# Kernel tuning notes

Measured on AMD Instinct MI355X. Metric: run time of the kernel, lower is better.

## Reference

```python
import jax, jax.numpy as jnp
import numpy as np
from jax import lax

K = 7          # neighborhood kernel size
NUM_HEADS = 4
EPS = 1e-5


def layernorm(x, w, b):
    mu = x.mean(-1, keepdims=True)
    var = ((x - mu) ** 2).mean(-1, keepdims=True)
    return (x - mu) * lax.rsqrt(var + EPS) * w + b


def window_idx(n, k):
    # NATTEN border behavior: window is shifted (not shrunk) at edges.
    start = jnp.clip(jnp.arange(n) - k // 2, 0, n - k)
    return start[:, None] + jnp.arange(k)  # [n, k]


def neighborhood_attention(x, qkv_w, qkv_b, rpb, proj_w, proj_b):
    B, H, W, C = x.shape
    nh, k = NUM_HEADS, K
    hd = C // nh
    scale = hd ** -0.5
    qkv = (x @ qkv_w + qkv_b).reshape(B, H, W, 3, nh, hd)
    q = jnp.transpose(qkv[:, :, :, 0], (0, 3, 1, 2, 4)) * scale  # [B,nh,H,W,hd]
    kk = jnp.transpose(qkv[:, :, :, 1], (0, 3, 1, 2, 4))
    vv = jnp.transpose(qkv[:, :, :, 2], (0, 3, 1, 2, 4))

    ri = window_idx(H, k)  # [H,k]
    ci = window_idx(W, k)  # [W,k]

    def gather(t):  # [B,nh,H,W,hd] -> [B,nh,H,W,k,k,hd]
        t = t[:, :, ri]           # [B,nh,H,k,W,hd]
        t = t[:, :, :, :, ci]     # [B,nh,H,k,W,k,hd]
        return jnp.transpose(t, (0, 1, 2, 4, 3, 5, 6))

    k_nb = gather(kk)
    v_nb = gather(vv).reshape(B, nh, H, W, k * k, hd)

    attn = jnp.einsum('bnhwd,bnhwijd->bnhwij', q, k_nb)  # [B,nh,H,W,k,k]

    # relative positional bias, rpb: [nh, 2k-1, 2k-1]
    br = ri - jnp.arange(H)[:, None] + (k - 1)  # [H,k] in [0, 2k-2]
    bc = ci - jnp.arange(W)[:, None] + (k - 1)  # [W,k]
    bias = rpb[:, br]                 # [nh,H,k,2k-1]
    bias = bias[:, :, :, bc]          # [nh,H,k,W,k]
    bias = jnp.transpose(bias, (0, 1, 3, 2, 4))  # [nh,H,W,k,k]

    attn = jax.nn.softmax((attn + bias[None]).reshape(B, nh, H, W, k * k), axis=-1)
    out = jnp.einsum('bnhwl,bnhwld->bnhwd', attn, v_nb)
    out = jnp.transpose(out, (0, 2, 3, 1, 4)).reshape(B, H, W, C)
    return out @ proj_w + proj_b


def mlp(x, w1, b1, w2, b2):
    return jax.nn.gelu(x @ w1 + b1, approximate=False) @ w2 + b2


def nat_block_forward(x, norm1_w, norm1_b, qkv_w, qkv_b, rpb, proj_w, proj_b,
                      norm2_w, norm2_b, fc1_w, fc1_b, fc2_w, fc2_b,
                      conv_w, dnorm_w, dnorm_b):
    depth = norm1_w.shape[0]
    for i in range(depth):
        h = layernorm(x, norm1_w[i], norm1_b[i])
        h = neighborhood_attention(h, qkv_w[i], qkv_b[i], rpb[i], proj_w[i], proj_b[i])
        x = x + h
        x = x + mlp(layernorm(x, norm2_w[i], norm2_b[i]),
                    fc1_w[i], fc1_b[i], fc2_w[i], fc2_b[i])
    # ConvDownsampler: 3x3 stride-2 conv (no bias) + LayerNorm, channels-last
    y = lax.conv_general_dilated(x, conv_w, (2, 2), ((1, 1), (1, 1)),
                                 dimension_numbers=('NHWC', 'HWIO', 'NHWC'))
    y = layernorm(y, dnorm_w, dnorm_b)
    return (y, x)


def setup_inputs() -> dict:
    key = jax.random.key(0)
    ks = jax.random.split(key, 12)
    B, H, W, C = 2, 56, 56, 128
    depth, nh, k = 2, NUM_HEADS, K
    hidden = 4 * C
    init = lambda kk, shape: jax.random.normal(kk, shape, jnp.float32) * 0.02
    return {
        'x': jax.random.normal(ks[0], (B, H, W, C), jnp.float32),
        'norm1_w': jnp.ones((depth, C), jnp.float32),
        'norm1_b': jnp.zeros((depth, C), jnp.float32),
        'qkv_w': init(ks[1], (depth, C, 3 * C)),
        'qkv_b': jnp.zeros((depth, 3 * C), jnp.float32),
        'rpb': init(ks[2], (depth, nh, 2 * k - 1, 2 * k - 1)),
        'proj_w': init(ks[3], (depth, C, C)),
        'proj_b': jnp.zeros((depth, C), jnp.float32),
        'norm2_w': jnp.ones((depth, C), jnp.float32),
        'norm2_b': jnp.zeros((depth, C), jnp.float32),
        'fc1_w': init(ks[4], (depth, C, hidden)),
        'fc1_b': jnp.zeros((depth, hidden), jnp.float32),
        'fc2_w': init(ks[5], (depth, hidden, C)),
        'fc2_b': jnp.zeros((depth, C), jnp.float32),
        'conv_w': init(ks[6], (3, 3, C, 2 * C)),
        'dnorm_w': jnp.ones((2 * C,), jnp.float32),
        'dnorm_b': jnp.zeros((2 * C,), jnp.float32),
    }


def reference(x, norm1_w, norm1_b, qkv_w, qkv_b, rpb, proj_w, proj_b,
              norm2_w, norm2_b, fc1_w, fc1_b, fc2_w, fc2_b,
              conv_w, dnorm_w, dnorm_b):
    return nat_block_forward(x, norm1_w, norm1_b, qkv_w, qkv_b, rpb, proj_w,
                             proj_b, norm2_w, norm2_b, fc1_w, fc1_b, fc2_w,
                             fc2_b, conv_w, dnorm_w, dnorm_b)
```

## Files before the change

kernel.cpp:

```cpp
#include <hip/hip_runtime.h>
#include <stdint.h>


typedef __attribute__((ext_vector_type(8))) short bf16x8;
typedef __attribute__((ext_vector_type(4))) float f32x4;

__device__ __forceinline__ float bf2f(uint16_t u) {
  union { uint32_t u; float f; } t;
  t.u = (uint32_t)u << 16;
  return t.f;
}
__device__ __forceinline__ uint16_t f2bf(float f) {
  union { float f; uint32_t u; } t;
  t.f = f;
  return (uint16_t)((t.u + 0x7FFFu + ((t.u >> 16) & 1u)) >> 16);
}

struct PrepArgs {
  const float* src[9];
  uint16_t* dst[9];
  int K[9], N[9];
  int cum[10];
};

__global__ __launch_bounds__(256) void prep_weights(PrepArgs a) {
  __shared__ float t[32][33];
  int bt = blockIdx.x;
  int j = 0;
#pragma unroll
  for (int u = 0; u < 9; ++u)
    if (bt >= a.cum[u + 1]) j = u + 1;
  int lt = bt - a.cum[j];
  const float* w = a.src[j];
  uint16_t* wt = a.dst[j];
  int K = a.K[j], N = a.N[j];
  int tn = N >> 5;
  int n0 = (lt % tn) * 32, k0 = (lt / tn) * 32;
  int tx = threadIdx.x & 31, ty = threadIdx.x >> 5;
#pragma unroll
  for (int r2 = 0; r2 < 32; r2 += 8)
    t[ty + r2][tx] = w[(size_t)(k0 + ty + r2) * N + n0 + tx];
  __syncthreads();
#pragma unroll
  for (int r2 = 0; r2 < 32; r2 += 8)
    wt[(size_t)(n0 + ty + r2) * K + k0 + tx] = f2bf(t[tx][ty + r2]);
}

__global__ __launch_bounds__(256) void ln256_kernel(const float* __restrict__ p0,
                                                    const float* __restrict__ p1,
                                                    const float* __restrict__ p2,
                                                    float* __restrict__ out,
                                                    const float* __restrict__ w,
                                                    const float* __restrict__ b) {
  int wave = threadIdx.x >> 6, lane = threadIdx.x & 63;
  int pix = blockIdx.x * 4 + wave;
  size_t base = (size_t)pix * 256 + lane * 4;
  float4 a0 = *(const float4*)(p0 + base);
  float4 a1 = *(const float4*)(p1 + base);
  float4 a2 = *(const float4*)(p2 + base);
  float4 v;
  v.x = a0.x + a1.x + a2.x;
  v.y = a0.y + a1.y + a2.y;
  v.z = a0.z + a1.z + a2.z;
  v.w = a0.w + a1.w + a2.w;
  float s = v.x + v.y + v.z + v.w;
  float s2 = v.x * v.x + v.y * v.y + v.z * v.z + v.w * v.w;
#pragma unroll
  for (int off = 32; off; off >>= 1) {
    s += __shfl_xor(s, off, 64);
    s2 += __shfl_xor(s2, off, 64);
  }
  float mu = s * (1.f / 256.f);
  float var = s2 * (1.f / 256.f) - mu * mu;
  float r = rsqrtf(var + 1e-5f);
  float4 wv = *(const float4*)(w + lane * 4);
  float4 bv = *(const float4*)(b + lane * 4);
  float4 o;
  o.x = (v.x - mu) * r * wv.x + bv.x;
  o.y = (v.y - mu) * r * wv.y + bv.y;
  o.z = (v.z - mu) * r * wv.z + bv.z;
  o.w = (v.w - mu) * r * wv.w + bv.w;
  *(float4*)(out + base) = o;
}

template <int KD, int ND, int ACT, int RES, int OUTB, int LNF>
__global__ __launch_bounds__(256) void mfma_gemm32(
    const uint16_t* __restrict__ A, const float* __restrict__ Af,
    const float* __restrict__ lnw, const float* __restrict__ lnb,
    const uint16_t* __restrict__ Wt, const float* __restrict__ bias,
    const float* __restrict__ res, float* __restrict__ outf,
    uint16_t* __restrict__ outb, float* __restrict__ outf2, int M) {
  __shared__ __align__(16) char smem[26112];
  uint16_t(*sA)[136] = (uint16_t(*)[136])smem;
  uint16_t(*sB)[136] = (uint16_t(*)[136])(smem + 8704);
  float(*sC)[68] = (float(*)[68])smem;

  int m0 = blockIdx.x * 32, n0 = blockIdx.y * 64;
  int tid = threadIdx.x, lane = tid & 63, wid = tid >> 6;
  int wr = (wid >> 1) * 16, wc = (wid & 1) * 32;
  int lc = lane & 15, g = lane >> 4;
  int lko = g * 8;

  f32x4 acc0 = {0.f, 0.f, 0.f, 0.f}, acc1 = acc0;

  constexpr int NCH = KD / 128;
#pragma unroll
  for (int c = 0; c < NCH; ++c) {
    if constexpr (LNF) {
      int r = tid >> 3, qt = tid & 7;
      const float4* xr = (const float4*)(Af + (size_t)(m0 + r) * 128 + qt * 16);
      float4 xv[4];
      float s = 0.f, s2 = 0.f;
#pragma unroll
      for (int u = 0; u < 4; ++u) {
        xv[u] = xr[u];
        s += xv[u].x + xv[u].y + xv[u].z + xv[u].w;
        s2 += xv[u].x * xv[u].x + xv[u].y * xv[u].y + xv[u].z * xv[u].z + xv[u].w * xv[u].w;
      }
      s += __shfl_xor(s, 1, 64);
      s += __shfl_xor(s, 2, 64);
      s += __shfl_xor(s, 4, 64);
      s2 += __shfl_xor(s2, 1, 64);
      s2 += __shfl_xor(s2, 2, 64);
      s2 += __shfl_xor(s2, 4, 64);
      float mu = s * (1.f / 128.f);
      float var = s2 * (1.f / 128.f) - mu * mu;
      float rstd = rsqrtf(var + 1e-5f);
      const float* lw = lnw + qt * 16;
      const float* lb = lnb + qt * 16;
      union { uint16_t us[8]; bf16x8 v; } tq[2];
#pragma unroll
      for (int u = 0; u < 4; ++u) {
        tq[u >> 1].us[(u & 1) * 4 + 0] = f2bf((xv[u].x - mu) * rstd * lw[u * 4 + 0] + lb[u * 4 + 0]);
        tq[u >> 1].us[(u & 1) * 4 + 1] = f2bf((xv[u].y - mu) * rstd * lw[u * 4 + 1] + lb[u * 4 + 1]);
        tq[u >> 1].us[(u & 1) * 4 + 2] = f2bf((xv[u].z - mu) * rstd * lw[u * 4 + 2] + lb[u * 4 + 2]);
        tq[u >> 1].us[(u & 1) * 4 + 3] = f2bf((xv[u].w - mu) * rstd * lw[u * 4 + 3] + lb[u * 4 + 3]);
      }
      *(bf16x8*)&sA[r][qt * 16] = tq[0].v;
      *(bf16x8*)&sA[r][qt * 16 + 8] = tq[1].v;
    } else {
#pragma unroll
      for (int it = 0; it < 2; ++it) {
        int chunk = tid + it * 256;
        int row = chunk >> 4, kc = (chunk & 15) * 8;
        *(bf16x8*)&sA[row][kc] =
            *(const bf16x8*)(A + (size_t)(m0 + row) * KD + c * 128 + kc);
      }
    }
#pragma unroll
    for (int it = 0; it < 4; ++it) {
      int chunk = tid + it * 256;
      int row = chunk >> 4, kc = (chunk & 15) * 8;
      *(bf16x8*)&sB[row][kc] =
          *(const bf16x8*)(Wt + (size_t)(n0 + row) * KD + c * 128 + kc);
    }
    __syncthreads();
#pragma unroll
    for (int kk = 0; kk < 128; kk += 32) {
      bf16x8 a0 = *(const bf16x8*)&sA[wr + lc][kk + lko];
      bf16x8 b0 = *(const bf16x8*)&sB[wc + lc][kk + lko];
      bf16x8 b1 = *(const bf16x8*)&sB[wc + 16 + lc][kk + lko];
      acc0 = __builtin_amdgcn_mfma_f32_16x16x32_bf16(a0, b0, acc0, 0, 0, 0);
      acc1 = __builtin_amdgcn_mfma_f32_16x16x32_bf16(a0, b1, acc1, 0, 0, 0);
    }
    __syncthreads();
  }

  {
    float bv0 = bias ? bias[n0 + wc + lc] : 0.f;
    float bv1 = bias ? bias[n0 + wc + lc + 16] : 0.f;
#pragma unroll
    for (int ni = 0; ni < 2; ++ni) {
      float bv = ni ? bv1 : bv0;
      f32x4 av = ni ? acc1 : acc0;
#pragma unroll
      for (int j = 0; j < 4; ++j) {
        float a = av[j] + bv;
        if (ACT) a = 0.5f * a * (1.f + erff(a * 0.70710678118654752f));
        sC[wr + g * 4 + j][wc + ni * 16 + lc] = a;
      }
    }
    __syncthreads();
    int r = tid >> 3, cs = (tid & 7) * 8;
    int grow = m0 + r;
    if (grow < M) {
      const float4* cp = (const float4*)&sC[r][cs];
      float4 c4[2] = {cp[0], cp[1]};
      if (RES) {
        const float4* rp = (const float4*)(res + (size_t)grow * ND + n0 + cs);
#pragma unroll
        for (int u = 0; u < 2; ++u) {
          float4 rv = rp[u];
          c4[u].x += rv.x; c4[u].y += rv.y; c4[u].z += rv.z; c4[u].w += rv.w;
        }
      }
      if (OUTB) {
        union { uint16_t us[8]; bf16x8 v; } t;
#pragma unroll
        for (int u = 0; u < 2; ++u) {
          t.us[u * 4 + 0] = f2bf(c4[u].x);
          t.us[u * 4 + 1] = f2bf(c4[u].y);
          t.us[u * 4 + 2] = f2bf(c4[u].z);
          t.us[u * 4 + 3] = f2bf(c4[u].w);
        }
        *(bf16x8*)(outb + (size_t)grow * ND + n0 + cs) = t.v;
      } else {
        float4* op = (float4*)(outf + (size_t)grow * ND + n0 + cs);
        op[0] = c4[0];
        op[1] = c4[1];
        if (outf2) {
          float4* op2 = (float4*)(outf2 + (size_t)grow * ND + n0 + cs);
          op2[0] = c4[0];
          op2[1] = c4[1];
        }
      }
    }
  }
}

template <int WQKV>
__global__ __launch_bounds__(512) void mlp_fused2(
    const uint16_t* __restrict__ att,
    const float* __restrict__ xin,
    const uint16_t* __restrict__ pwt,
    const float* __restrict__ pb,
    const float* __restrict__ n2w, const float* __restrict__ n2b,
    const uint16_t* __restrict__ f1wt,
    const float* __restrict__ f1b,
    const uint16_t* __restrict__ f2wt,
    const float* __restrict__ f2b,
    float* __restrict__ xout,
    float* __restrict__ out2,
    const float* __restrict__ n1w, const float* __restrict__ n1b,
    const uint16_t* __restrict__ qwt,
    const float* __restrict__ qb,
    uint16_t* __restrict__ qkvout) {
  __shared__ __align__(16) uint16_t sW[128][136];
  __shared__ __align__(16) uint16_t sA[16][136];
  __shared__ __align__(16) float sY[16][132];
  __shared__ __align__(16) char sHraw[16640];
  uint16_t(*sH)[520] = (uint16_t(*)[520])sHraw;
  float(*sC)[132] = (float(*)[132])sHraw;

  const f32x4 fz = {0.f, 0.f, 0.f, 0.f};
  int m0 = blockIdx.x * 16;
  int tid = threadIdx.x;
  int lane = tid & 63, wid = tid >> 6;
  int lc = lane & 15, g = lane >> 4;
  int rr = tid >> 5, cc = tid & 31;

  float4 rx = *(const float4*)(xin + (size_t)(m0 + rr) * 128 + cc * 4);

  if (tid < 256) {
    int r = tid >> 4, q = tid & 15;
    *(bf16x8*)&sA[r][q * 8] = *(const bf16x8*)(att + (size_t)(m0 + r) * 128 + q * 8);
  }
#pragma unroll
  for (int it = 0; it < 4; ++it) {
    int chunk = tid + it * 512;
    int row = chunk >> 4, q = chunk & 15;
    *(bf16x8*)&sW[row][q * 8] = *(const bf16x8*)(pwt + (size_t)row * 128 + q * 8);
  }
  __syncthreads();

  {
    f32x4 acc = fz;
#pragma unroll
    for (int ks = 0; ks < 4; ++ks) {
      bf16x8 a = *(const bf16x8*)&sA[lc][ks * 32 + g * 8];
      bf16x8 b = *(const bf16x8*)&sW[wid * 16 + lc][ks * 32 + g * 8];
      acc = __builtin_amdgcn_mfma_f32_16x16x32_bf16(a, b, acc, 0, 0, 0);
    }
    float bv = pb[wid * 16 + lc];
#pragma unroll
    for (int j = 0; j < 4; ++j) sY[g * 4 + j][wid * 16 + lc] = acc[j] + bv;
  }
  __syncthreads();

  {
    float4 sv = *(const float4*)&sY[rr][cc * 4];
    float4 y;
    y.x = sv.x + rx.x; y.y = sv.y + rx.y; y.z = sv.z + rx.z; y.w = sv.w + rx.w;
    float s = y.x + y.y + y.z + y.w;
    float s2 = y.x * y.x + y.y * y.y + y.z * y.z + y.w * y.w;
#pragma unroll
    for (int off = 1; off < 32; off <<= 1) {
      s += __shfl_xor(s, off, 64);
      s2 += __shfl_xor(s2, off, 64);
    }
    float mu = s * (1.f / 128.f);
    float var = s2 * (1.f / 128.f) - mu * mu;
    float rstd = rsqrtf(var + 1e-5f);
    *(float4*)&sY[rr][cc * 4] = y;
    float4 lw = *(const float4*)(n2w + cc * 4);
    float4 lb = *(const float4*)(n2b + cc * 4);
    ushort4 nv;
    nv.x = f2bf((y.x - mu) * rstd * lw.x + lb.x);
    nv.y = f2bf((y.y - mu) * rstd * lw.y + lb.y);
    nv.z = f2bf((y.z - mu) * rstd * lw.z + lb.z);
    nv.w = f2bf((y.w - mu) * rstd * lw.w + lb.w);
    *(ushort4*)&sA[rr][cc * 4] = nv;
  }
  __syncthreads();

#pragma unroll 1
  for (int ch = 0; ch < 4; ++ch) {
#pragma unroll
    for (int it = 0; it < 4; ++it) {
      int chunk = tid + it * 512;
      int row = chunk >> 4, q = chunk & 15;
      *(bf16x8*)&sW[row][q * 8] =
          *(const bf16x8*)(f1wt + (size_t)(ch * 128 + row) * 128 + q * 8);
    }
    __syncthreads();
    f32x4 acc = fz;
#pragma unroll
    for (int ks = 0; ks < 4; ++ks) {
      bf16x8 a = *(const bf16x8*)&sA[lc][ks * 32 + g * 8];
      bf16x8 b = *(const bf16x8*)&sW[wid * 16 + lc][ks * 32 + g * 8];
      acc = __builtin_amdgcn_mfma_f32_16x16x32_bf16(a, b, acc, 0, 0, 0);
    }
    int col = ch * 128 + wid * 16 + lc;
    float bv = f1b[col];
#pragma unroll
    for (int j = 0; j < 4; ++j) {
      float h = acc[j] + bv;
      h = 0.5f * h * (1.f + erff(h * 0.70710678118654752f));
      sH[g * 4 + j][col] = f2bf(h);
    }
    __syncthreads();
  }

  f32x4 acc2 = fz;
#pragma unroll 1
  for (int ch = 0; ch < 4; ++ch) {
#pragma unroll
    for (int it = 0; it < 4; ++it) {
      int chunk = tid + it * 512;
      int row = chunk >> 4, q = chunk & 15;
      *(bf16x8*)&sW[row][q * 8] =
          *(const bf16x8*)(f2wt + (size_t)row * 512 + ch * 128 + q * 8);
    }
    __syncthreads();
#pragma unroll
    for (int ks = 0; ks < 4; ++ks) {
      bf16x8 a = *(const bf16x8*)&sH[lc][ch * 128 + ks * 32 + g * 8];
      bf16x8 b = *(const bf16x8*)&sW[wid * 16 + lc][ks * 32 + g * 8];
      acc2 = __builtin_amdgcn_mfma_f32_16x16x32_bf16(a, b, acc2, 0, 0, 0);
    }
    __syncthreads();
  }

  {
    int col = wid * 16 + lc;
    float bv = f2b[col];
#pragma unroll
    for (int j = 0; j < 4; ++j) sC[g * 4 + j][col] = acc2[j] + bv;
  }
  __syncthreads();

  {
    float4 cv = *(const float4*)&sC[rr][cc * 4];
    float4 yv = *(const float4*)&sY[rr][cc * 4];
    float4 o;
    o.x = cv.x + yv.x; o.y = cv.y + yv.y; o.z = cv.z + yv.z; o.w = cv.w + yv.w;
    *(float4*)(xout + (size_t)(m0 + rr) * 128 + cc * 4) = o;
    if (out2) *(float4*)(out2 + (size_t)(m0 + rr) * 128 + cc * 4) = o;
    if constexpr (WQKV) {
      float s = o.x + o.y + o.z + o.w;
      float s2 = o.x * o.x + o.y * o.y + o.z * o.z + o.w * o.w;
#pragma unroll
      for (int off = 1; off < 32; off <<= 1) {
        s += __shfl_xor(s, off, 64);
        s2 += __shfl_xor(s2, off, 64);
      }
      float mu = s * (1.f / 128.f);
      float var = s2 * (1.f / 128.f) - mu * mu;
      float rstd = rsqrtf(var + 1e-5f);
      float4 lw = *(const float4*)(n1w + cc * 4);
      float4 lb = *(const float4*)(n1b + cc * 4);
      ushort4 nv;
      nv.x = f2bf((o.x - mu) * rstd * lw.x + lb.x);
      nv.y = f2bf((o.y - mu) * rstd * lw.y + lb.y);
      nv.z = f2bf((o.z - mu) * rstd * lw.z + lb.z);
      nv.w = f2bf((o.w - mu) * rstd * lw.w + lb.w);
      *(ushort4*)&sA[rr][cc * 4] = nv;
    }
  }

  if constexpr (WQKV) {
#pragma unroll 1
    for (int ch = 0; ch < 3; ++ch) {
#pragma unroll
      for (int it = 0; it < 4; ++it) {
        int chunk = tid + it * 512;
        int row = chunk >> 4, q = chunk & 15;
        *(bf16x8*)&sW[row][q * 8] =
            *(const bf16x8*)(qwt + (size_t)(ch * 128 + row) * 128 + q * 8);
      }
      __syncthreads();
      f32x4 acc = fz;
#pragma unroll
      for (int ks = 0; ks < 4; ++ks) {
        bf16x8 a = *(const bf16x8*)&sA[lc][ks * 32 + g * 8];
        bf16x8 b = *(const bf16x8*)&sW[wid * 16 + lc][ks * 32 + g * 8];
        acc = __builtin_amdgcn_mfma_f32_16x16x32_bf16(a, b, acc, 0, 0, 0);
      }
      int col = ch * 128 + wid * 16 + lc;
      float bv = qb[col];
#pragma unroll
      for (int j = 0; j < 4; ++j) sH[g * 4 + j][col] = f2bf(acc[j] + bv);
      __syncthreads();
    }
    for (int idx = tid; idx < 1536; idx += 512) {
      int row = idx / 96, colc = (idx % 96) * 4;
      *(ushort4*)(qkvout + (size_t)(m0 + row) * 384 + colc) =
          *(const ushort4*)&sH[row][colc];
    }
  }
}

#define KSWZ(row, colbytes) (((row) * 64 + (colbytes)) ^ (((row) & 7) << 4))

__global__ __launch_bounds__(128) void natten_mfma(const uint16_t* __restrict__ qkv,
                                                   const float* __restrict__ rpb,
                                                   uint16_t* __restrict__ out) {
  __shared__ uint16_t s_k[144 * 32];
  __shared__ uint16_t s_vt[32][168];
  __shared__ uint16_t s_p[32][168];
  __shared__ float s_rpb[169];

  int tid = threadIdx.x;
  int blk = blockIdx.x;
  int bh = blk & 7, tile = blk >> 3;
  int b = bh >> 2, head = bh & 3;
  int ti = tile / 7, tj = tile % 7;
  int i0 = ti * 4, j0 = tj * 8;
  int rbase = min(max(i0 - 3, 0), 46);
  int cbase = min(max(j0 - 3, 0), 42);

  const bf16x8 bz = {0, 0, 0, 0, 0, 0, 0, 0};
  const f32x4 fz = {0.f, 0.f, 0.f, 0.f};

  if (tid < 16)
    *(bf16x8*)((char*)s_k + KSWZ(140 + (tid >> 2), (tid & 3) * 16)) = bz;
  for (int idx = tid; idx < 640; idx += 128) s_vt[idx & 31][140 + (idx >> 5)] = 0;
  for (int idx = tid; idx < 512; idx += 128) s_p[idx & 31][144 + (idx >> 5)] = 0;
  for (int idx = tid; idx < 560; idx += 128) {
    int pos = idx >> 2, ch = (idx & 3) * 8;
    int r = rbase + pos / 14, c = cbase + pos % 14;
    const uint16_t* base = qkv + ((size_t)(b * 3136 + r * 56 + c)) * 384 + head * 32 + ch;
    bf16x8 kv = *(const bf16x8*)(base + 128);
    bf16x8 vv = *(const bf16x8*)(base + 256);
    *(bf16x8*)((char*)s_k + KSWZ(pos, ch * 2)) = kv;
#pragma unroll
    for (int e = 0; e < 8; ++e) s_vt[ch + e][pos] = (uint16_t)vv[e];
  }
  for (int idx = tid; idx < 169; idx += 128) s_rpb[idx] = rpb[head * 169 + idx];
  __syncthreads();

  int lane = tid & 63, wq = tid >> 6;
  int lc = lane & 15, g = lane >> 4;
  int q0 = wq * 16;

  int pA = q0 + lc;
  int piA = i0 + (pA >> 3), pjA = j0 + (pA & 7);
  bf16x8 qfrag =
      *(const bf16x8*)(qkv + ((size_t)(b * 3136 + piA * 56 + pjA)) * 384 + head * 32 + g * 8);

  f32x4 S[9];
#pragma unroll
  for (int t = 0; t < 9; ++t) {
    bf16x8 kfrag = *(const bf16x8*)((char*)s_k + KSWZ(t * 16 + lc, g * 16));
    S[t] = __builtin_amdgcn_mfma_f32_16x16x32_bf16(qfrag, kfrag, fz, 0, 0, 0);
  }

  int qi = wq * 2 + (g >> 1);
  int i = i0 + qi;
  int a = min(max(i - 3, 0), 49) - rbase;
  int brc = 6 - (i0 - rbase) - qi;
  int bj[4], bcc[4];
#pragma unroll
  for (int jj = 0; jj < 4; ++jj) {
    int qj = 4 * (g & 1) + jj;
    int j = j0 + qj;
    bj[jj] = min(max(j - 3, 0), 49) - cbase;
    bcc[jj] = 6 - (j0 - cbase) - qj;
  }

  float mx[4] = {-1e30f, -1e30f, -1e30f, -1e30f};
  int kr = (lc >= 14) ? 1 : 0;
  int kc = lc - 14 * kr;
#pragma unroll
  for (int t = 0; t < 9; ++t) {
    bool vr = (kr >= a) && (kr <= a + 6);
    int brrow = (kr + brc) * 13;
#pragma unroll
    for (int jj = 0; jj < 4; ++jj) {
      float sv = S[t][jj] * 0.17677669529663687f;
      bool v = vr && (kc >= bj[jj]) && (kc <= bj[jj] + 6);
      int bidx = v ? (brrow + kc + bcc[jj]) : 0;
      float val = v ? (sv + s_rpb[bidx]) : -1e30f;
      S[t][jj] = val;
      mx[jj] = fmaxf(mx[jj], val);
    }
    kr += 1;
    kc += 2;
    if (kc >= 14) { kc -= 14; kr += 1; }
  }
#pragma unroll
  for (int jj = 0; jj < 4; ++jj) {
#pragma unroll
    for (int off = 1; off < 16; off <<= 1) mx[jj] = fmaxf(mx[jj], __shfl_xor(mx[jj], off, 64));
  }

  float sm[4] = {0.f, 0.f, 0.f, 0.f};
#pragma unroll
  for (int t = 0; t < 9; ++t) {
#pragma unroll
    for (int jj = 0; jj < 4; ++jj) {
      float e = __expf(S[t][jj] - mx[jj]);
      sm[jj] += e;
      s_p[q0 + g * 4 + jj][t * 16 + lc] = f2bf(e);
    }
  }
#pragma unroll
  for (int jj = 0; jj < 4; ++jj) {
#pragma unroll
    for (int off = 1; off < 16; off <<= 1) sm[jj] += __shfl_xor(sm[jj], off, 64);
    sm[jj] = 1.f / sm[jj];
  }

  __syncthreads();

  f32x4 O[2] = {fz, fz};
#pragma unroll
  for (int ks = 0; ks < 5; ++ks) {
    bf16x8 pa = *(const bf16x8*)&s_p[q0 + lc][ks * 32 + g * 8];
#pragma unroll
    for (int dt = 0; dt < 2; ++dt) {
      bf16x8 vb = *(const bf16x8*)&s_vt[dt * 16 + lc][ks * 32 + g * 8];
      O[dt] = __builtin_amdgcn_mfma_f32_16x16x32_bf16(pa, vb, O[dt], 0, 0, 0);
    }
  }

#pragma unroll
  for (int jj = 0; jj < 4; ++jj) {
    int q = q0 + g * 4 + jj;
    int pi = i0 + (q >> 3), pj = j0 + (q & 7);
    size_t ob = ((size_t)(b * 3136 + pi * 56 + pj)) * 128 + head * 32;
    out[ob + lc] = f2bf(O[0][jj] * sm[jj]);
    out[ob + 16 + lc] = f2bf(O[1][jj] * sm[jj]);
  }
}

__global__ __launch_bounds__(256) void conv_gemm32(const float* __restrict__ x,
                                                   const uint16_t* __restrict__ Wt,
                                                   float* __restrict__ parts) {
  __shared__ __align__(16) char smem[26112];
  uint16_t(*sA)[136] = (uint16_t(*)[136])smem;
  uint16_t(*sB)[136] = (uint16_t(*)[136])(smem + 8704);
  float(*sC)[68] = (float(*)[68])smem;

  int m0 = blockIdx.x * 32, n0 = blockIdx.y * 64, kh = blockIdx.z;
  float* part = parts + (size_t)kh * 1568 * 256;
  int tid = threadIdx.x, lane = tid & 63, wid = tid >> 6;
  int wr = (wid >> 1) * 16, wc = (wid & 1) * 32;
  int lc = lane & 15, g = lane >> 4;
  int lko = g * 8;

  f32x4 acc0 = {0.f, 0.f, 0.f, 0.f}, acc1 = acc0;

  int r = tid >> 3, qt = tid & 7;
  int opix = m0 + r;
  int ow = opix % 28, oh = (opix / 28) % 28, bb = opix / 784;
  int ih = 2 * oh - 1 + kh;
  bool rowok = (ih >= 0) && (ih < 56);

#pragma unroll
  for (int kwc = 0; kwc < 3; ++kwc) {
    int iw = 2 * ow - 1 + kwc;
    float4 xv[4] = {{0.f, 0.f, 0.f, 0.f}, {0.f, 0.f, 0.f, 0.f},
                    {0.f, 0.f, 0.f, 0.f}, {0.f, 0.f, 0.f, 0.f}};
    if (rowok && iw >= 0 && iw < 56) {
      const float4* p =
          (const float4*)(x + (size_t)((bb * 56 + ih) * 56 + iw) * 128 + qt * 16);
#pragma unroll
      for (int u = 0; u < 4; ++u) xv[u] = p[u];
    }
    union { uint16_t us[8]; bf16x8 v; } tq[2];
#pragma unroll
    for (int u = 0; u < 4; ++u) {
      tq[u >> 1].us[(u & 1) * 4 + 0] = f2bf(xv[u].x);
      tq[u >> 1].us[(u & 1) * 4 + 1] = f2bf(xv[u].y);
      tq[u >> 1].us[(u & 1) * 4 + 2] = f2bf(xv[u].z);
      tq[u >> 1].us[(u & 1) * 4 + 3] = f2bf(xv[u].w);
    }
    *(bf16x8*)&sA[r][qt * 16] = tq[0].v;
    *(bf16x8*)&sA[r][qt * 16 + 8] = tq[1].v;
#pragma unroll
    for (int it = 0; it < 4; ++it) {
      int chunk = tid + it * 256;
      int row = chunk >> 4, kc = (chunk & 15) * 8;
      *(bf16x8*)&sB[row][kc] =
          *(const bf16x8*)(Wt + (size_t)(n0 + row) * 1152 + kh * 384 + kwc * 128 + kc);
    }
    __syncthreads();
#pragma unroll
    for (int kk = 0; kk < 128; kk += 32) {
      bf16x8 a0 = *(const bf16x8*)&sA[wr + lc][kk + lko];
      bf16x8 b0 = *(const bf16x8*)&sB[wc + lc][kk + lko];
      bf16x8 b1 = *(const bf16x8*)&sB[wc + 16 + lc][kk + lko];
      acc0 = __builtin_amdgcn_mfma_f32_16x16x32_bf16(a0, b0, acc0, 0, 0, 0);
      acc1 = __builtin_amdgcn_mfma_f32_16x16x32_bf16(a0, b1, acc1, 0, 0, 0);
    }
    __syncthreads();
  }

#pragma unroll
  for (int ni = 0; ni < 2; ++ni) {
    f32x4 av = ni ? acc1 : acc0;
#pragma unroll
    for (int j = 0; j < 4; ++j) sC[wr + g * 4 + j][wc + ni * 16 + lc] = av[j];
  }
  __syncthreads();
  int rr = tid >> 3, cs = (tid & 7) * 8;
  int grow = m0 + rr;
  if (grow < 1568) {
    const float4* cp = (const float4*)&sC[rr][cs];
    float4* op = (float4*)(part + (size_t)grow * 256 + n0 + cs);
    op[0] = cp[0];
    op[1] = cp[1];
  }
}

extern "C" void kernel_launch(void* const* d_in, const int* in_sizes, int n_in,
                              void* d_out, int out_size, void* d_ws, size_t ws_size,
                              hipStream_t stream) {
  const float* x    = (const float*)d_in[0];
  const float* n1w  = (const float*)d_in[1];
  const float* n1b  = (const float*)d_in[2];
  const float* qkvw = (const float*)d_in[3];
  const float* qkvb = (const float*)d_in[4];
  const float* rpb  = (const float*)d_in[5];
  const float* pw   = (const float*)d_in[6];
  const float* pb   = (const float*)d_in[7];
  const float* n2w  = (const float*)d_in[8];
  const float* n2b  = (const float*)d_in[9];
  const float* f1w  = (const float*)d_in[10];
  const float* f1b  = (const float*)d_in[11];
  const float* f2w  = (const float*)d_in[12];
  const float* f2b  = (const float*)d_in[13];
  const float* cw   = (const float*)d_in[14];
  const float* dnw  = (const float*)d_in[15];
  const float* dnb  = (const float*)d_in[16];
  float* out = (float*)d_out;

  char* wsb = (char*)d_ws;
  float*    xbuf    = (float*)(wsb + 0);
  uint16_t* qkv_b   = (uint16_t*)(wsb + 3211264);
  uint16_t* att_b   = (uint16_t*)(wsb + 8028160);
  float*    parts   = (float*)(wsb + 16056320);
  uint16_t* wts     = (uint16_t*)(wsb + 20873216);
  uint16_t* qkvwt = wts;
  uint16_t* pwt   = wts + 98304;
  uint16_t* f1wt  = wts + 131072;
  uint16_t* f2wt  = wts + 262144;
  uint16_t* cwt   = wts + 393216;

  PrepArgs pa;
  pa.src[0] = qkvw;         pa.dst[0] = qkvwt;          pa.K[0] = 128; pa.N[0] = 384;
  pa.src[1] = qkvw + 49152; pa.dst[1] = qkvwt + 49152;  pa.K[1] = 128; pa.N[1] = 384;
  pa.src[2] = pw;           pa.dst[2] = pwt;            pa.K[2] = 128; pa.N[2] = 128;
  pa.src[3] = pw + 16384;   pa.dst[3] = pwt + 16384;    pa.K[3] = 128; pa.N[3] = 128;
  pa.src[4] = f1w;          pa.dst[4] = f1wt;           pa.K[4] = 128; pa.N[4] = 512;
  pa.src[5] = f1w + 65536;  pa.dst[5] = f1wt + 65536;   pa.K[5] = 128; pa.N[5] = 512;
  pa.src[6] = f2w;          pa.dst[6] = f2wt;           pa.K[6] = 512; pa.N[6] = 128;
  pa.src[7] = f2w + 65536;  pa.dst[7] = f2wt + 65536;   pa.K[7] = 512; pa.N[7] = 128;
  pa.src[8] = cw;           pa.dst[8] = cwt;            pa.K[8] = 1152; pa.N[8] = 256;
  int cums[10] = {0, 48, 96, 112, 128, 192, 256, 320, 384, 672};
  for (int u = 0; u < 10; ++u) pa.cum[u] = cums[u];
  prep_weights<<<672, 256, 0, stream>>>(pa);

  mfma_gemm32<128, 384, 0, 0, 1, 1><<<dim3(196, 6), 256, 0, stream>>>(
      nullptr, x, n1w, n1b, qkvwt, qkvb, nullptr, nullptr, qkv_b, nullptr, 6272);
  natten_mfma<<<784, 128, 0, stream>>>(qkv_b, rpb, att_b);
  mlp_fused2<1><<<392, 512, 0, stream>>>(
      att_b, x, pwt, pb, n2w, n2b, f1wt, f1b, f2wt, f2b, xbuf, nullptr,
      n1w + 128, n1b + 128, qkvwt + 49152, qkvb + 384, qkv_b);
  natten_mfma<<<784, 128, 0, stream>>>(qkv_b, rpb + 676, att_b);
  mlp_fused2<0><<<392, 512, 0, stream>>>(
      att_b, xbuf, pwt + 16384, pb + 128, n2w + 128, n2b + 128,
      f1wt + 65536, f1b + 512, f2wt + 65536, f2b + 128, xbuf, out + 401408,
      nullptr, nullptr, nullptr, nullptr, nullptr);

  conv_gemm32<<<dim3(49, 4, 3), 256, 0, stream>>>(xbuf, cwt, parts);
  ln256_kernel<<<392, 256, 0, stream>>>(parts, parts + 401408, parts + 802816, out, dnw, dnb);
}
```

Baseline: 83.62 us.

## Read MLP weight fragments directly from global memory instead of staging in LDS

Result: slower. 95.01 us (+13.6%).

```diff
diff --git a/kernel.cpp b/kernel.cpp
--- a/kernel.cpp
+++ b/kernel.cpp
@@ -219,7 +219,7 @@
 }
 
 template <int WQKV>
-__global__ __launch_bounds__(512) void mlp_fused2(
+__global__ __launch_bounds__(512) void mlp_fused3(
     const uint16_t* __restrict__ att,
     const float* __restrict__ xin,
     const uint16_t* __restrict__ pwt,
@@ -235,7 +235,6 @@
     const uint16_t* __restrict__ qwt,
     const float* __restrict__ qb,
     uint16_t* __restrict__ qkvout) {
-  __shared__ __align__(16) uint16_t sW[128][136];
   __shared__ __align__(16) uint16_t sA[16][136];
   __shared__ __align__(16) float sY[16][132];
   __shared__ __align__(16) char sHraw[16640];
@@ -255,12 +254,6 @@
     int r = tid >> 4, q = tid & 15;
     *(bf16x8*)&sA[r][q * 8] = *(const bf16x8*)(att + (size_t)(m0 + r) * 128 + q * 8);
   }
-#pragma unroll
-  for (int it = 0; it < 4; ++it) {
-    int chunk = tid + it * 512;
-    int row = chunk >> 4, q = chunk & 15;
-    *(bf16x8*)&sW[row][q * 8] = *(const bf16x8*)(pwt + (size_t)row * 128 + q * 8);
-  }
   __syncthreads();
 
   {
@@ -268,7 +261,7 @@
 #pragma unroll
     for (int ks = 0; ks < 4; ++ks) {
       bf16x8 a = *(const bf16x8*)&sA[lc][ks * 32 + g * 8];
-      bf16x8 b = *(const bf16x8*)&sW[wid * 16 + lc][ks * 32 + g * 8];
+      bf16x8 b = *(const bf16x8*)(pwt + (size_t)(wid * 16 + lc) * 128 + ks * 32 + g * 8);
       acc = __builtin_amdgcn_mfma_f32_16x16x32_bf16(a, b, acc, 0, 0, 0);
     }
     float bv = pb[wid * 16 + lc];
@@ -303,21 +296,14 @@
   }
   __syncthreads();
 
-#pragma unroll 1
+#pragma unroll
   for (int ch = 0; ch < 4; ++ch) {
-#pragma unroll
-    for (int it = 0; it < 4; ++it) {
-      int chunk = tid + it * 512;
-      int row = chunk >> 4, q = chunk & 15;
-      *(bf16x8*)&sW[row][q * 8] =
-          *(const bf16x8*)(f1wt + (size_t)(ch * 128 + row) * 128 + q * 8);
-    }
-    __syncthreads();
     f32x4 acc = fz;
 #pragma unroll
     for (int ks = 0; ks < 4; ++ks) {
       bf16x8 a = *(const bf16x8*)&sA[lc][ks * 32 + g * 8];
-      bf16x8 b = *(const bf16x8*)&sW[wid * 16 + lc][ks * 32 + g * 8];
+      bf16x8 b = *(const bf16x8*)(f1wt + (size_t)(ch * 128 + wid * 16 + lc) * 128 +
+                                  ks * 32 + g * 8);
       acc = __builtin_amdgcn_mfma_f32_16x16x32_bf16(a, b, acc, 0, 0, 0);
     }
     int col = ch * 128 + wid * 16 + lc;
@@ -328,28 +314,17 @@
       h = 0.5f * h * (1.f + erff(h * 0.70710678118654752f));
       sH[g * 4 + j][col] = f2bf(h);
     }
-    __syncthreads();
-  }
+  }
+  __syncthreads();
 
   f32x4 acc2 = fz;
-#pragma unroll 1
-  for (int ch = 0; ch < 4; ++ch) {
-#pragma unroll
-    for (int it = 0; it < 4; ++it) {
-      int chunk = tid + it * 512;
-      int row = chunk >> 4, q = chunk & 15;
-      *(bf16x8*)&sW[row][q * 8] =
-          *(const bf16x8*)(f2wt + (size_t)row * 512 + ch * 128 + q * 8);
-    }
-    __syncthreads();
-#pragma unroll
-    for (int ks = 0; ks < 4; ++ks) {
-      bf16x8 a = *(const bf16x8*)&sH[lc][ch * 128 + ks * 32 + g * 8];
-      bf16x8 b = *(const bf16x8*)&sW[wid * 16 + lc][ks * 32 + g * 8];
-      acc2 = __builtin_amdgcn_mfma_f32_16x16x32_bf16(a, b, acc2, 0, 0, 0);
-    }
-    __syncthreads();
-  }
+#pragma unroll
+  for (int ks = 0; ks < 16; ++ks) {
+    bf16x8 a = *(const bf16x8*)&sH[lc][ks * 32 + g * 8];
+    bf16x8 b = *(const bf16x8*)(f2wt + (size_t)(wid * 16 + lc) * 512 + ks * 32 + g * 8);
+    acc2 = __builtin_amdgcn_mfma_f32_16x16x32_bf16(a, b, acc2, 0, 0, 0);
+  }
+  __syncthreads();
 
   {
     int col = wid * 16 + lc;
@@ -389,29 +364,23 @@
   }
 
   if constexpr (WQKV) {
-#pragma unroll 1
+    __syncthreads();
+#pragma unroll
     for (int ch = 0; ch < 3; ++ch) {
-#pragma unroll
-      for (int it = 0; it < 4; ++it) {
-        int chunk = tid + it * 512;
-        int row = chunk >> 4, q = chunk & 15;
-        *(bf16x8*)&sW[row][q * 8] =
-            *(const bf16x8*)(qwt + (size_t)(ch * 128 + row) * 128 + q * 8);
-      }
-      __syncthreads();
       f32x4 acc = fz;
 #pragma unroll
       for (int ks = 0; ks < 4; ++ks) {
         bf16x8 a = *(const bf16x8*)&sA[lc][ks * 32 + g * 8];
-        bf16x8 b = *(const bf16x8*)&sW[wid * 16 + lc][ks * 32 + g * 8];
+        bf16x8 b = *(const bf16x8*)(qwt + (size_t)(ch * 128 + wid * 16 + lc) * 128 +
+                                    ks * 32 + g * 8);
         acc = __builtin_amdgcn_mfma_f32_16x16x32_bf16(a, b, acc, 0, 0, 0);
       }
       int col = ch * 128 + wid * 16 + lc;
       float bv = qb[col];
 #pragma unroll
       for (int j = 0; j < 4; ++j) sH[g * 4 + j][col] = f2bf(acc[j] + bv);
-      __syncthreads();
-    }
+    }
+    __syncthreads();
     for (int idx = tid; idx < 1536; idx += 512) {
       int row = idx / 96, colc = (idx % 96) * 4;
       *(ushort4*)(qkvout + (size_t)(m0 + row) * 384 + colc) =
@@ -685,11 +654,11 @@
   mfma_gemm32<128, 384, 0, 0, 1, 1><<<dim3(196, 6), 256, 0, stream>>>(
       nullptr, x, n1w, n1b, qkvwt, qkvb, nullptr, nullptr, qkv_b, nullptr, 6272);
   natten_mfma<<<784, 128, 0, stream>>>(qkv_b, rpb, att_b);
-  mlp_fused2<1><<<392, 512, 0, stream>>>(
+  mlp_fused3<1><<<392, 512, 0, stream>>>(
       att_b, x, pwt, pb, n2w, n2b, f1wt, f1b, f2wt, f2b, xbuf, nullptr,
       n1w + 128, n1b + 128, qkvwt + 49152, qkvb + 384, qkv_b);
   natten_mfma<<<784, 128, 0, stream>>>(qkv_b, rpb + 676, att_b);
-  mlp_fused2<0><<<392, 512, 0, stream>>>(
+  mlp_fused3<0><<<392, 512, 0, stream>>>(
       att_b, xbuf, pwt + 16384, pb + 128, n2w + 128, n2b + 128,
       f1wt + 65536, f1b + 512, f2wt + 65536, f2b + 128, xbuf, out + 401408,
       nullptr, nullptr, nullptr, nullptr, nullptr);
```
